# Kernel optimization log

Measured on AMD Instinct MI355X. Metric: run time of the kernel, lower is better.

Reference implementation:

```python
import jax, jax.numpy as jnp
import numpy as np

B, L, D, H, F, NL = 112, 128, 768, 12, 3072, 3
E = D // H  # head dim = 64
BN_EPS = 1e-5


def _bn(x, gamma, beta):
    # torch BatchNorm1d applied on x.permute(0,2,1): per-channel (d_model) stats over batch+seq
    mean = jnp.mean(x, axis=(0, 1), keepdims=True)
    var = jnp.var(x, axis=(0, 1), keepdims=True)
    return (x - mean) * jax.lax.rsqrt(var + BN_EPS) * gamma + beta


def setup_inputs() -> dict:
    key = jax.random.key(0)
    ks = jax.random.split(key, 10)
    s = 0.02
    inp = {
        "x": jax.random.normal(ks[0], (B, L, D), jnp.float32),
        "attn_bias": jax.random.normal(ks[1], (B, L, L, H), jnp.float32) * 0.1,
        "Wq": jax.random.normal(ks[2], (NL, D, D), jnp.float32) * s,
        "bq": jnp.zeros((NL, D), jnp.float32),
        "Wk": jax.random.normal(ks[3], (NL, D, D), jnp.float32) * s,
        "bk": jnp.zeros((NL, D), jnp.float32),
        "Wv": jax.random.normal(ks[4], (NL, D, D), jnp.float32) * s,
        "bv": jnp.zeros((NL, D), jnp.float32),
        "Wo": jax.random.normal(ks[5], (NL, D, D), jnp.float32) * s,
        "bo": jnp.zeros((NL, D), jnp.float32),
        "W1": jax.random.normal(ks[6], (NL, F, D), jnp.float32) * s,  # conv1 k=1 == Linear
        "b1": jnp.zeros((NL, F), jnp.float32),
        "W2": jax.random.normal(ks[7], (NL, D, F), jnp.float32) * s,  # conv2 k=1 == Linear
        "b2": jnp.zeros((NL, D), jnp.float32),
        "g1": jnp.ones((NL, D), jnp.float32),
        "be1": jnp.zeros((NL, D), jnp.float32),
        "g2": jnp.ones((NL, D), jnp.float32),
        "be2": jnp.zeros((NL, D), jnp.float32),
        "gf": jnp.ones((D,), jnp.float32),
        "bef": jnp.zeros((D,), jnp.float32),
    }
    return inp


def reference(x, attn_bias, Wq, bq, Wk, bk, Wv, bv, Wo, bo,
              W1, b1, W2, b2, g1, be1, g2, be2, gf, bef):
    scale = 1.0 / float(np.sqrt(E))
    bias_bhls = jnp.transpose(attn_bias, (0, 3, 1, 2))  # [B,H,L,S]
    for l in range(NL):
        q = (x @ Wq[l].T + bq[l]).reshape(B, L, H, E)
        k = (x @ Wk[l].T + bk[l]).reshape(B, L, H, E)
        v = (x @ Wv[l].T + bv[l]).reshape(B, L, H, E)
        scores = jnp.einsum('blhe,bshe->bhls', q, k)  # O(L^2) score tensor
        A = jax.nn.softmax(scores * scale + bias_bhls, axis=-1)
        V = jnp.einsum('bhls,bshd->blhd', A, v).reshape(B, L, D)
        new_x = V @ Wo[l].T + bo[l]
        x = _bn(x + new_x, g1[l], be1[l])
        y = jax.nn.gelu(x @ W1[l].T + b1[l], approximate=False)
        y = y @ W2[l].T + b2[l]
        x = _bn(x + y, g2[l], be2[l])
    return _bn(x, gf, bef)  # Encoder final BatchNorm1d(d_model)
```

## Files before the change

kernel.cpp:

```cpp
#include <hip/hip_runtime.h>

#define NB 112
#define SEQ 128
#define DM 768
#define NH 12
#define HD 64
#define FF 3072
#define NLAYER 3
#define MTOK (NB*SEQ)
#define QKVN (3*DM)
#define HEADTOT (NB*NH)
#define QSZ ((size_t)HEADTOT*SEQ*HD)

typedef unsigned short u16;
typedef __attribute__((ext_vector_type(8))) short short8;
typedef __attribute__((ext_vector_type(4))) float f32x4;
typedef __attribute__((ext_vector_type(4))) unsigned short us4;

__device__ __forceinline__ u16 f2bf(float f){
  unsigned u = __builtin_bit_cast(unsigned, f);
  u += 0x7FFFu + ((u >> 16) & 1u);
  return (u16)(u >> 16);
}
__device__ __forceinline__ float bf2f(u16 b){
  unsigned u = ((unsigned)b) << 16;
  return __builtin_bit_cast(float, u);
}
__device__ __forceinline__ unsigned cvt_pk_bf16(float lo, float hi){
  unsigned r;
  asm("v_cvt_pk_bf16_f32 %0, %1, %2" : "=v"(r) : "v"(lo), "v"(hi));
  return r;
}
__device__ __forceinline__ float gelu_t(float x){
  const float t = -1.5957691216057308f * x * __builtin_fmaf(0.044715f, x*x, 1.0f);
  return __fdividef(x, 1.0f + __expf(t));
}

__device__ __forceinline__ void gl_lds16(const void* g, void* l){
  __builtin_amdgcn_global_load_lds((const __attribute__((address_space(1))) unsigned*)g,
                                   (__attribute__((address_space(3))) unsigned*)l, 16, 0, 0);
}

template<int EPI>
__global__ __launch_bounds__(512, 2)
void gemm_bt(const u16* __restrict__ A, const u16* __restrict__ W,
             const float* __restrict__ bias, u16* __restrict__ obf,
             float* __restrict__ of32, const u16* __restrict__ res,
             float* __restrict__ p1, float* __restrict__ p2,
             int M, int N, int K, int Nt, int TPB)
{
  __shared__ __align__(16) char smem[131072];
  const int tid = threadIdx.x;
  const int w = tid >> 6, lane = tid & 63;
  const int wm = w >> 2, wn = w & 3;
  const int fr = lane & 15, fg = lane >> 4;
  const int fko = fg * 8;
  const int grid = gridDim.x;
  const int q8 = grid >> 3, r8 = grid & 7;
  const int xcd = blockIdx.x & 7, pos = blockIdx.x >> 3;
  const int start = xcd < r8 ? xcd * (q8 + 1) : r8 * (q8 + 1) + (xcd - r8) * q8;
  const int swz = start + pos;
  const int nt = K >> 6;
  const int tot = TPB * nt;
  const int l3 = lane >> 3;
  const int k16s = ((lane & 7) ^ l3) * 8;
  int rowAK[2][2], rowBK[2][2];
  #pragma unroll
  for (int mh = 0; mh < 2; mh++)
    #pragma unroll
    for (int j = 0; j < 2; j++)
      rowAK[mh][j] = (mh*64 + j*128 + w*8 + l3) * K;
  #pragma unroll
  for (int h = 0; h < 2; h++)
    #pragma unroll
    for (int j = 0; j < 2; j++)
      rowBK[h][j] = (h*128 + (w + j*8)*8 + l3) * K;

  auto stA2 = [&](int bb, int mh, int soff) {
    const u16* g0 = A + (size_t)soff + rowAK[mh][0] + k16s;
    const u16* g1 = A + (size_t)soff + rowAK[mh][1] + k16s;
    char* d = smem + bb*65536 + (mh*64 + w*8)*128;
    gl_lds16(g0, d);
    gl_lds16(g1, d + 16384);
  };
  auto stB2 = [&](int bb, int h, int soff) {
    const u16* g0 = W + (size_t)soff + rowBK[h][0] + k16s;
    const u16* g1 = W + (size_t)soff + rowBK[h][1] + k16s;
    char* d = smem + bb*65536 + 32768 + (h*128 + w*8)*128;
    gl_lds16(g0, d);
    gl_lds16(g1, d + 8192);
  };
  const int axor = (fr & 7) << 4;
  auto rdA2 = [&](int bb, int mh, int kh, int mf) -> short8 {
    const int row = wm*128 + mh*64 + mf*16 + fr;
    return *(const short8*)(smem + bb*65536 + row*128 + (((kh*32 + fko)*2) ^ axor));
  };
  auto rdB2 = [&](int bb, int kh, int nf) -> short8 {
    const int row = wn*64 + nf*16 + fr;
    return *(const short8*)(smem + bb*65536 + 32768 + row*128 + (((kh*32 + fko)*2) ^ axor));
  };
  auto coord = [&](int r, int& bm, int& bn) {
    const int lin = swz * TPB + r;
    const int mI = lin / Nt;
    bm = mI * 256; bn = (lin - mI * Nt) * 256;
  };

  f32x4 acc[8][4] = {};

  auto epi = [&](int bm, int bn) {
    float bs[4] = {0,0,0,0}, bq[4] = {0,0,0,0};
    #pragma unroll
    for (int mi = 0; mi < 8; mi++) {
      #pragma unroll
      for (int ni = 0; ni < 4; ni++) {
        const int c = bn + wn*64 + ni*16 + fr;
        const int r0 = bm + wm*128 + (mi>>2)*64 + (mi&3)*16 + fg*4;
        const float bc = bias[c];
        float v[4];
        #pragma unroll
        for (int j = 0; j < 4; j++) v[j] = acc[mi][ni][j] + bc;
        if constexpr (EPI == 1) {
          #pragma unroll
          for (int j = 0; j < 4; j++) v[j] = gelu_t(v[j]);
          const unsigned p01 = cvt_pk_bf16(v[0], v[1]);
          const unsigned p23 = cvt_pk_bf16(v[2], v[3]);
          u16* d = obf + (size_t)r0 * N + c;
          d[0] = (u16)p01; d[N] = (u16)(p01 >> 16);
          d[2*N] = (u16)p23; d[3*N] = (u16)(p23 >> 16);
        } else if constexpr (EPI == 2) {
          #pragma unroll
          for (int j = 0; j < 4; j++) {
            const float y = v[j] + bf2f(res[(size_t)(r0+j) * N + c]);
            of32[(size_t)(r0+j) * N + c] = y;
            bs[ni] += y; bq[ni] += y * y;
          }
        } else {
          const int which = c / DM;
          const int cc = c - which * DM;
          const int hh = cc >> 6, e = cc & 63;
          const int bb = r0 >> 7, l = r0 & 127;
          const unsigned p01 = cvt_pk_bf16(v[0], v[1]);
          const unsigned p23 = cvt_pk_bf16(v[2], v[3]);
          u16* d = obf + (size_t)which * QSZ + ((size_t)(bb*NH + hh) * SEQ + l) * HD + e;
          d[0] = (u16)p01; d[HD] = (u16)(p01 >> 16);
          d[2*HD] = (u16)p23; d[3*HD] = (u16)(p23 >> 16);
        }
        acc[mi][ni] = (f32x4){0.f, 0.f, 0.f, 0.f};
      }
    }
    if constexpr (EPI == 2) {
      const int mIdx = bm >> 8;
      #pragma unroll
      for (int ni = 0; ni < 4; ni++) {
        float s = bs[ni], qq = bq[ni];
        s  += __shfl_xor(s, 16);  s  += __shfl_xor(s, 32);
        qq += __shfl_xor(qq, 16); qq += __shfl_xor(qq, 32);
        if (fg == 0) {
          const int c = bn + wn*64 + ni*16 + fr;
          p1[(mIdx*2 + wm) * N + c] = s;
          p2[(mIdx*2 + wm) * N + c] = qq;
        }
      }
    }
  };

  int r0t = 0, kt0 = 0, bm0, bn0; coord(0, bm0, bn0);
  int r1 = 0, kt1 = 1, bm1 = bm0, bn1 = bn0;
  int r2 = 0, kt2 = 2, bm2 = bm0;
  if (kt2 >= nt) { kt2 -= nt; r2 = 1; int d; if (r2 < TPB) coord(r2, bm2, d); }

  stA2(0, 0, bm0*K); stA2(0, 1, bm0*K);
  stB2(0, 0, bn0*K); stB2(0, 1, bn0*K);
  if (tot > 1) stA2(1, 0, bm1*K + kt1*64);
  asm volatile("s_waitcnt vmcnt(2)" ::: "memory");
  __builtin_amdgcn_s_barrier();

  short8 a0[4], a1[4], bk0[4], bk1[4];
  for (int it = 0; it < tot; ++it) {
    const int bufc = it & 1, nb = bufc ^ 1;
    const bool st1 = (it + 1 < tot), st2 = (it + 2 < tot);
    const int sB1 = bn1*K + kt1*64;
    const int sA1 = bm1*K + kt1*64;
    const int sA2 = bm2*K + kt2*64;
    #pragma unroll
    for (int i = 0; i < 4; i++) a0[i] = rdA2(bufc, 0, 0, i);
    #pragma unroll
    for (int i = 0; i < 4; i++) a1[i] = rdA2(bufc, 0, 1, i);
    #pragma unroll
    for (int i = 0; i < 4; i++) bk0[i] = rdB2(bufc, 0, i);
    #pragma unroll
    for (int i = 0; i < 4; i++) bk1[i] = rdB2(bufc, 1, i);
    if (st1) { stB2(nb, 0, sB1); stB2(nb, 1, sB1); }
    __builtin_amdgcn_s_barrier();
    asm volatile("s_waitcnt lgkmcnt(0)" ::: "memory");
    __builtin_amdgcn_sched_barrier(0);
    __builtin_amdgcn_s_setprio(1);
    #pragma unroll
    for (int mi = 0; mi < 4; mi++)
      #pragma unroll
      for (int ni = 0; ni < 4; ni++)
        acc[mi][ni] = __builtin_amdgcn_mfma_f32_16x16x32_bf16(a0[mi], bk0[ni], acc[mi][ni], 0, 0, 0);
    #pragma unroll
    for (int mi = 0; mi < 4; mi++)
      #pragma unroll
      for (int ni = 0; ni < 4; ni++)
        acc[mi][ni] = __builtin_amdgcn_mfma_f32_16x16x32_bf16(a1[mi], bk1[ni], acc[mi][ni], 0, 0, 0);
    __builtin_amdgcn_s_setprio(0);
    if (st1) { asm volatile("s_waitcnt vmcnt(4)" ::: "memory"); }
    else     { asm volatile("s_waitcnt vmcnt(0)" ::: "memory"); }
    __builtin_amdgcn_s_barrier();
    #pragma unroll
    for (int i = 0; i < 4; i++) a0[i] = rdA2(bufc, 1, 0, i);
    #pragma unroll
    for (int i = 0; i < 4; i++) a1[i] = rdA2(bufc, 1, 1, i);
    if (st2) stA2(bufc, 0, sA2);
    if (st1) stA2(nb, 1, sA1);
    __builtin_amdgcn_s_barrier();
    asm volatile("s_waitcnt lgkmcnt(0)" ::: "memory");
    __builtin_amdgcn_sched_barrier(0);
    __builtin_amdgcn_s_setprio(1);
    #pragma unroll
    for (int mi = 0; mi < 4; mi++)
      #pragma unroll
      for (int ni = 0; ni < 4; ni++)
        acc[4+mi][ni] = __builtin_amdgcn_mfma_f32_16x16x32_bf16(a0[mi], bk0[ni], acc[4+mi][ni], 0, 0, 0);
    #pragma unroll
    for (int mi = 0; mi < 4; mi++)
      #pragma unroll
      for (int ni = 0; ni < 4; ni++)
        acc[4+mi][ni] = __builtin_amdgcn_mfma_f32_16x16x32_bf16(a1[mi], bk1[ni], acc[4+mi][ni], 0, 0, 0);
    __builtin_amdgcn_s_setprio(0);
    if (st2)      { asm volatile("s_waitcnt vmcnt(4)" ::: "memory"); }
    else if (st1) { asm volatile("s_waitcnt vmcnt(2)" ::: "memory"); }
    __builtin_amdgcn_s_barrier();
    if (kt0 == nt - 1) {
      epi(bm0, bn0);
      kt0 = 0; r0t++;
      if (r0t < TPB) coord(r0t, bm0, bn0);
    } else kt0++;
    kt1++; if (kt1 == nt) { kt1 = 0; r1++; if (r1 < TPB) coord(r1, bm1, bn1); }
    kt2++; if (kt2 == nt) { kt2 = 0; r2++; if (r2 < TPB) { int d; coord(r2, bm2, d); } }
  }
}

__global__ __launch_bounds__(256)
void attn_kernel(const u16* __restrict__ qkvb, const u16* __restrict__ biasT,
                 u16* __restrict__ ab)
{
  const int h = blockIdx.x, b = blockIdx.y;
  const int tid = threadIdx.x, w = tid >> 6, lane = tid & 63;
  const int bh = b * NH + h;
  const u16* qp = qkvb + (size_t)bh * SEQ * HD;
  const u16* kp = qkvb + QSZ + (size_t)bh * SEQ * HD;
  const u16* vp = qkvb + 2 * QSZ + (size_t)bh * SEQ * HD;
  __shared__ __align__(16) u16 vT[HD * 136];
  __shared__ __align__(16) u16 P[SEQ * 136];
  {
    const int s = tid & 127, half = tid >> 7;
    #pragma unroll
    for (int rr = 0; rr < 4; rr++) {
      const int e0 = half * 32 + rr * 8;
      short8 v8 = *(const short8*)&vp[s * HD + e0];
      #pragma unroll
      for (int j = 0; j < 8; j++) vT[(e0 + j) * 136 + s] = (u16)v8[j];
    }
  }
  const int fr = lane & 15, fg = lane >> 4;
  f32x4 sacc[2][8] = {};
  #pragma unroll
  for (int ks = 0; ks < 2; ks++) {
    const int k0 = ks * 32 + fg * 8;
    short8 qf[2], kf[8];
    #pragma unroll
    for (int mi = 0; mi < 2; mi++) qf[mi] = *(const short8*)&qp[(w*32 + mi*16 + fr) * HD + k0];
    #pragma unroll
    for (int ni = 0; ni < 8; ni++) kf[ni] = *(const short8*)&kp[(ni*16 + fr) * HD + k0];
    #pragma unroll
    for (int mi = 0; mi < 2; mi++)
      #pragma unroll
      for (int ni = 0; ni < 8; ni++)
        sacc[mi][ni] = __builtin_amdgcn_mfma_f32_16x16x32_bf16(qf[mi], kf[ni], sacc[mi][ni], 0, 0, 0);
  }
  const u16* bt = biasT + (size_t)bh * SEQ * SEQ;
  #pragma unroll
  for (int mi = 0; mi < 2; mi++) {
    #pragma unroll
    for (int j = 0; j < 4; j++) {
      const int l = w*32 + mi*16 + fg*4 + j;
      float vals[8];
      float mx = -1e30f;
      #pragma unroll
      for (int ni = 0; ni < 8; ni++) {
        vals[ni] = sacc[mi][ni][j] * 0.125f + bf2f(bt[l * SEQ + ni*16 + fr]);
        mx = fmaxf(mx, vals[ni]);
      }
      #pragma unroll
      for (int d = 1; d < 16; d <<= 1) mx = fmaxf(mx, __shfl_xor(mx, d));
      float sum = 0.f;
      #pragma unroll
      for (int ni = 0; ni < 8; ni++) { vals[ni] = __expf(vals[ni] - mx); sum += vals[ni]; }
      #pragma unroll
      for (int d = 1; d < 16; d <<= 1) sum += __shfl_xor(sum, d);
      const float inv = 1.0f / sum;
      #pragma unroll
      for (int ni = 0; ni < 8; ni++) P[l * 136 + ni*16 + fr] = f2bf(vals[ni] * inv);
    }
  }
  __syncthreads();
  f32x4 oacc[2][4] = {};
  #pragma unroll
  for (int ss = 0; ss < 4; ss++) {
    const int s0 = ss * 32 + fg * 8;
    short8 pf[2], vf[4];
    #pragma unroll
    for (int mi = 0; mi < 2; mi++) pf[mi] = *(const short8*)&P[(w*32 + mi*16 + fr) * 136 + s0];
    #pragma unroll
    for (int ei = 0; ei < 4; ei++) vf[ei] = *(const short8*)&vT[(ei*16 + fr) * 136 + s0];
    #pragma unroll
    for (int mi = 0; mi < 2; mi++)
      #pragma unroll
      for (int ei = 0; ei < 4; ei++)
        oacc[mi][ei] = __builtin_amdgcn_mfma_f32_16x16x32_bf16(pf[mi], vf[ei], oacc[mi][ei], 0, 0, 0);
  }
  #pragma unroll
  for (int mi = 0; mi < 2; mi++)
    #pragma unroll
    for (int ei = 0; ei < 4; ei++)
      #pragma unroll
      for (int j = 0; j < 4; j++) {
        const int r = b * SEQ + w*32 + mi*16 + fg*4 + j;
        const int c = h * HD + ei*16 + fr;
        ab[(size_t)r * DM + c] = f2bf(oacc[mi][ei][j]);
      }
}

template<bool FINAL>
__global__ __launch_bounds__(256)
void bn_final(const float* __restrict__ p1, const float* __restrict__ p2,
              const float* __restrict__ ga, const float* __restrict__ be,
              const float* __restrict__ gb, const float* __restrict__ beb,
              float* __restrict__ sc, float* __restrict__ sh)
{
  const int c = blockIdx.x * 256 + threadIdx.x;
  float s = 0, q = 0;
  for (int i = 0; i < 112; i++) { s += p1[i * DM + c]; q += p2[i * DM + c]; }
  const float mean = s * (1.0f / MTOK);
  const float var = q * (1.0f / MTOK) - mean * mean;
  const float rstd = rsqrtf(var + 1e-5f);
  if constexpr (!FINAL) {
    const float g = ga[c] * rstd;
    sc[c] = g;
    sh[c] = be[c] - mean * g;
  } else {
    const float sc2 = ga[c] * rstd;
    const float sh2 = be[c] - mean * sc2;
    const float varf = sc2 * sc2 * var;
    const float meanf = sc2 * mean + sh2;
    const float scf = gb[c] * rsqrtf(varf + 1e-5f);
    const float shf = beb[c] - meanf * scf;
    sc[c] = scf * sc2;
    sh[c] = scf * sh2 + shf;
  }
}

template<int MODE>
__global__ __launch_bounds__(256)
void bn_apply(const float* __restrict__ xi, const float* __restrict__ sc,
              const float* __restrict__ sh, float* __restrict__ xo, u16* __restrict__ xb)
{
  const int i = blockIdx.x * 256 + threadIdx.x;
  const int c0 = (i % (DM / 8)) * 2;
  float4 v0 = ((const float4*)xi)[i*2];
  float4 v1 = ((const float4*)xi)[i*2 + 1];
  const float4 s0 = ((const float4*)sc)[c0];
  const float4 s1 = ((const float4*)sc)[c0 + 1];
  const float4 h0 = ((const float4*)sh)[c0];
  const float4 h1 = ((const float4*)sh)[c0 + 1];
  float y0x = __builtin_fmaf(v0.x, s0.x, h0.x), y0y = __builtin_fmaf(v0.y, s0.y, h0.y);
  float y0z = __builtin_fmaf(v0.z, s0.z, h0.z), y0w = __builtin_fmaf(v0.w, s0.w, h0.w);
  float y1x = __builtin_fmaf(v1.x, s1.x, h1.x), y1y = __builtin_fmaf(v1.y, s1.y, h1.y);
  float y1z = __builtin_fmaf(v1.z, s1.z, h1.z), y1w = __builtin_fmaf(v1.w, s1.w, h1.w);
  if constexpr (MODE == 1) {
    ((float4*)xo)[i*2]     = (float4){y0x, y0y, y0z, y0w};
    ((float4*)xo)[i*2 + 1] = (float4){y1x, y1y, y1z, y1w};
  } else {
    short8 r;
    unsigned pA = cvt_pk_bf16(y0x, y0y), pB = cvt_pk_bf16(y0z, y0w);
    unsigned pC = cvt_pk_bf16(y1x, y1y), pD = cvt_pk_bf16(y1z, y1w);
    r[0] = (short)(u16)pA; r[1] = (short)(u16)(pA >> 16);
    r[2] = (short)(u16)pB; r[3] = (short)(u16)(pB >> 16);
    r[4] = (short)(u16)pC; r[5] = (short)(u16)(pC >> 16);
    r[6] = (short)(u16)pD; r[7] = (short)(u16)(pD >> 16);
    *(short8*)&xb[(size_t)i * 8] = r;
  }
}

__global__ __launch_bounds__(256)
void conv_bf16(const float* __restrict__ s, u16* __restrict__ d, int n8)
{
  const int i = blockIdx.x * 256 + threadIdx.x;
  if (i >= n8) return;
  float4 v0 = ((const float4*)s)[i*2];
  float4 v1 = ((const float4*)s)[i*2 + 1];
  short8 r;
  unsigned pA = cvt_pk_bf16(v0.x, v0.y), pB = cvt_pk_bf16(v0.z, v0.w);
  unsigned pC = cvt_pk_bf16(v1.x, v1.y), pD = cvt_pk_bf16(v1.z, v1.w);
  r[0] = (short)(u16)pA; r[1] = (short)(u16)(pA >> 16);
  r[2] = (short)(u16)pB; r[3] = (short)(u16)(pB >> 16);
  r[4] = (short)(u16)pC; r[5] = (short)(u16)(pC >> 16);
  r[6] = (short)(u16)pD; r[7] = (short)(u16)(pD >> 16);
  *(short8*)&d[(size_t)i * 8] = r;
}

__global__ __launch_bounds__(256)
void conv_qkvw(const float* __restrict__ wq, const float* __restrict__ wk,
               const float* __restrict__ wv, u16* __restrict__ d)
{
  const int i = blockIdx.x * 256 + threadIdx.x;
  const int per = QKVN * DM / 8;
  const int l = i / per;
  const int rem = i - l * per;
  const int r = rem / (DM / 8);
  const int cv = rem - r * (DM / 8);
  const float* srcrow;
  if (r < DM)          srcrow = wq + ((size_t)l * DM + r) * DM;
  else if (r < 2 * DM) srcrow = wk + ((size_t)l * DM + (r - DM)) * DM;
  else                 srcrow = wv + ((size_t)l * DM + (r - 2 * DM)) * DM;
  float4 v0 = ((const float4*)srcrow)[cv*2];
  float4 v1 = ((const float4*)srcrow)[cv*2 + 1];
  short8 o;
  unsigned pA = cvt_pk_bf16(v0.x, v0.y), pB = cvt_pk_bf16(v0.z, v0.w);
  unsigned pC = cvt_pk_bf16(v1.x, v1.y), pD = cvt_pk_bf16(v1.z, v1.w);
  o[0] = (short)(u16)pA; o[1] = (short)(u16)(pA >> 16);
  o[2] = (short)(u16)pB; o[3] = (short)(u16)(pB >> 16);
  o[4] = (short)(u16)pC; o[5] = (short)(u16)(pC >> 16);
  o[6] = (short)(u16)pD; o[7] = (short)(u16)(pD >> 16);
  *(short8*)&d[(size_t)i * 8] = o;
}

__global__ __launch_bounds__(256)
void conv_bias_qkv(const float* __restrict__ bq, const float* __restrict__ bk,
                   const float* __restrict__ bv, float* __restrict__ d)
{
  const int i = blockIdx.x * 256 + threadIdx.x;
  const int l = i / QKVN;
  const int r = i - l * QKVN;
  float v;
  if (r < DM)          v = bq[l * DM + r];
  else if (r < 2 * DM) v = bk[l * DM + r - DM];
  else                 v = bv[l * DM + r - 2 * DM];
  d[i] = v;
}

__global__ __launch_bounds__(256)
void bias_tr(const float* __restrict__ src, u16* __restrict__ dst)
{
  const int l = blockIdx.x, b = blockIdx.y;
  __shared__ float row[SEQ * NH];
  const float* s = src + ((size_t)b * SEQ + l) * SEQ * NH;
  for (int i = threadIdx.x; i < SEQ * NH; i += 256) row[i] = s[i];
  __syncthreads();
  for (int i = threadIdx.x; i < SEQ * NH; i += 256) {
    const int h = i >> 7, ss = i & 127;
    dst[((size_t)(b * NH + h) * SEQ + l) * SEQ + ss] = f2bf(row[ss * NH + h]);
  }
}

extern "C" void kernel_launch(void* const* d_in, const int* in_sizes, int n_in,
                              void* d_out, int out_size, void* d_ws, size_t ws_size,
                              hipStream_t stream)
{
  const float* x    = (const float*)d_in[0];
  const float* abia = (const float*)d_in[1];
  const float* Wq   = (const float*)d_in[2];
  const float* bq   = (const float*)d_in[3];
  const float* Wk   = (const float*)d_in[4];
  const float* bk   = (const float*)d_in[5];
  const float* Wv   = (const float*)d_in[6];
  const float* bv   = (const float*)d_in[7];
  const float* Wo   = (const float*)d_in[8];
  const float* bo   = (const float*)d_in[9];
  const float* W1   = (const float*)d_in[10];
  const float* b1   = (const float*)d_in[11];
  const float* W2   = (const float*)d_in[12];
  const float* b2   = (const float*)d_in[13];
  const float* g1   = (const float*)d_in[14];
  const float* be1  = (const float*)d_in[15];
  const float* g2   = (const float*)d_in[16];
  const float* be2  = (const float*)d_in[17];
  const float* gf   = (const float*)d_in[18];
  const float* bef  = (const float*)d_in[19];
  float* out = (float*)d_out;

  char* ws = (char*)d_ws;
  size_t off = 0;
  auto alloc = [&](size_t n) -> char* {
    char* p = ws + off;
    off = (off + n + 255) & ~(size_t)255;
    return p;
  };
  u16*  wqkv  = (u16*)alloc((size_t)3 * QKVN * DM * 2);
  u16*  wo    = (u16*)alloc((size_t)3 * DM * DM * 2);
  u16*  w1    = (u16*)alloc((size_t)3 * FF * DM * 2);
  u16*  w2    = (u16*)alloc((size_t)3 * DM * FF * 2);
  float* bqkv = (float*)alloc((size_t)3 * QKVN * 4);
  u16*  xb    = (u16*)alloc((size_t)MTOK * DM * 2);
  u16*  ab    = (u16*)alloc((size_t)MTOK * DM * 2);
  u16*  big   = (u16*)alloc((size_t)MTOK * FF * 2);
  u16*  biasT = (u16*)alloc((size_t)HEADTOT * SEQ * SEQ * 2);
  float* p1   = (float*)alloc((size_t)112 * DM * 4);
  float* p2   = (float*)alloc((size_t)112 * DM * 4);
  float* sc   = (float*)alloc(DM * 4);
  float* sh   = (float*)alloc(DM * 4);
  if (off > ws_size) return;

  conv_qkvw<<<2592, 256, 0, stream>>>(Wq, Wk, Wv, wqkv);
  conv_bf16<<<864, 256, 0, stream>>>(Wo, wo, 3 * DM * DM / 8);
  conv_bf16<<<3456, 256, 0, stream>>>(W1, w1, 3 * FF * DM / 8);
  conv_bf16<<<3456, 256, 0, stream>>>(W2, w2, 3 * DM * FF / 8);
  conv_bias_qkv<<<27, 256, 0, stream>>>(bq, bk, bv, bqkv);
  bias_tr<<<dim3(SEQ, NB), 256, 0, stream>>>(abia, biasT);
  conv_bf16<<<MTOK * DM / 8 / 256, 256, 0, stream>>>(x, xb, MTOK * DM / 8);

  auto gemm = [&](int epi, const u16* Ap, const u16* Wp, const float* bp,
                  u16* ob, float* o32, const u16* rs, int M, int N, int K) {
    const int Nt = N / 256;
    const int tiles = (M / 256) * Nt;
    const int tpb = (tiles + 255) / 256;
    const int grid = tiles / tpb;
    if (epi == 1)
      gemm_bt<1><<<grid, 512, 0, stream>>>(Ap, Wp, bp, ob, o32, rs, p1, p2, M, N, K, Nt, tpb);
    else if (epi == 2)
      gemm_bt<2><<<grid, 512, 0, stream>>>(Ap, Wp, bp, ob, o32, rs, p1, p2, M, N, K, Nt, tpb);
    else
      gemm_bt<3><<<grid, 512, 0, stream>>>(Ap, Wp, bp, ob, o32, rs, p1, p2, M, N, K, Nt, tpb);
  };

  for (int l = 0; l < NLAYER; l++) {
    gemm(3, xb, wqkv + (size_t)l * QKVN * DM, bqkv + l * QKVN, big, nullptr, nullptr,
         MTOK, QKVN, DM);
    attn_kernel<<<dim3(NH, NB), 256, 0, stream>>>(big, biasT, ab);
    gemm(2, ab, wo + (size_t)l * DM * DM, bo + l * DM, nullptr, out, xb,
         MTOK, DM, DM);
    bn_final<false><<<3, 256, 0, stream>>>(p1, p2, g1 + l * DM, be1 + l * DM,
                                           nullptr, nullptr, sc, sh);
    bn_apply<0><<<MTOK * DM / 8 / 256, 256, 0, stream>>>(out, sc, sh, nullptr, xb);
    gemm(1, xb, w1 + (size_t)l * FF * DM, b1 + l * FF, big, nullptr, nullptr,
         MTOK, FF, DM);
    gemm(2, big, w2 + (size_t)l * DM * FF, b2 + l * DM, nullptr, out, xb,
         MTOK, DM, FF);
    if (l < NLAYER - 1) {
      bn_final<false><<<3, 256, 0, stream>>>(p1, p2, g2 + l * DM, be2 + l * DM,
                                             nullptr, nullptr, sc, sh);
      bn_apply<0><<<MTOK * DM / 8 / 256, 256, 0, stream>>>(out, sc, sh, nullptr, xb);
    } else {
      bn_final<true><<<3, 256, 0, stream>>>(p1, p2, g2 + l * DM, be2 + l * DM,
                                            gf, bef, sc, sh);
      bn_apply<1><<<MTOK * DM / 8 / 256, 256, 0, stream>>>(out, sc, sh, out, nullptr);
    }
  }
}
```

Baseline: 1.146 ms.

## Triple-buffer A tiles in GEMM LDS to cut per-iteration barriers

Restructures the GEMM main loop from a double-buffered scheme with split A half-tile loads and three barriers per iteration to a three-slot A ring plus two-slot B ring, issuing full-tile async loads once per iteration with one barrier. LDS grows to 160KB, so launch bounds drop to one block of 512 threads per CU. This aims to remove barrier stalls and deepen prefetch, at the cost of halving occupancy and less latency hiding across blocks.

New measurement: 1.132 ms (median of 2 runs). No clear change (-1.2%).

```diff
diff --git a/kernel.cpp b/kernel.cpp
--- a/kernel.cpp
+++ b/kernel.cpp
@@ -42,14 +42,14 @@
 }
 
 template<int EPI>
-__global__ __launch_bounds__(512, 2)
+__global__ __launch_bounds__(512, 1)
 void gemm_bt(const u16* __restrict__ A, const u16* __restrict__ W,
              const float* __restrict__ bias, u16* __restrict__ obf,
              float* __restrict__ of32, const u16* __restrict__ res,
              float* __restrict__ p1, float* __restrict__ p2,
              int M, int N, int K, int Nt, int TPB)
 {
-  __shared__ __align__(16) char smem[131072];
+  __shared__ __align__(16) char smem[163840];
   const int tid = threadIdx.x;
   const int w = tid >> 6, lane = tid & 63;
   const int wm = w >> 2, wn = w & 3;
@@ -76,28 +76,30 @@
     for (int j = 0; j < 2; j++)
       rowBK[h][j] = (h*128 + (w + j*8)*8 + l3) * K;
 
-  auto stA2 = [&](int bb, int mh, int soff) {
-    const u16* g0 = A + (size_t)soff + rowAK[mh][0] + k16s;
-    const u16* g1 = A + (size_t)soff + rowAK[mh][1] + k16s;
-    char* d = smem + bb*65536 + (mh*64 + w*8)*128;
-    gl_lds16(g0, d);
-    gl_lds16(g1, d + 16384);
-  };
-  auto stB2 = [&](int bb, int h, int soff) {
-    const u16* g0 = W + (size_t)soff + rowBK[h][0] + k16s;
-    const u16* g1 = W + (size_t)soff + rowBK[h][1] + k16s;
-    char* d = smem + bb*65536 + 32768 + (h*128 + w*8)*128;
-    gl_lds16(g0, d);
-    gl_lds16(g1, d + 8192);
+  auto stA = [&](int s, int soff) {
+    #pragma unroll
+    for (int mh = 0; mh < 2; mh++) {
+      char* d = smem + s*32768 + (mh*64 + w*8)*128;
+      gl_lds16(A + (size_t)soff + rowAK[mh][0] + k16s, d);
+      gl_lds16(A + (size_t)soff + rowAK[mh][1] + k16s, d + 16384);
+    }
+  };
+  auto stB = [&](int s, int soff) {
+    #pragma unroll
+    for (int h = 0; h < 2; h++) {
+      char* d = smem + 98304 + s*32768 + (h*128 + w*8)*128;
+      gl_lds16(W + (size_t)soff + rowBK[h][0] + k16s, d);
+      gl_lds16(W + (size_t)soff + rowBK[h][1] + k16s, d + 8192);
+    }
   };
   const int axor = (fr & 7) << 4;
-  auto rdA2 = [&](int bb, int mh, int kh, int mf) -> short8 {
+  auto rdA2 = [&](int s, int mh, int kh, int mf) -> short8 {
     const int row = wm*128 + mh*64 + mf*16 + fr;
-    return *(const short8*)(smem + bb*65536 + row*128 + (((kh*32 + fko)*2) ^ axor));
-  };
-  auto rdB2 = [&](int bb, int kh, int nf) -> short8 {
+    return *(const short8*)(smem + s*32768 + row*128 + (((kh*32 + fko)*2) ^ axor));
+  };
+  auto rdB2 = [&](int s, int kh, int nf) -> short8 {
     const int row = wn*64 + nf*16 + fr;
-    return *(const short8*)(smem + bb*65536 + 32768 + row*128 + (((kh*32 + fko)*2) ^ axor));
+    return *(const short8*)(smem + 98304 + s*32768 + row*128 + (((kh*32 + fko)*2) ^ axor));
   };
   auto coord = [&](int r, int& bm, int& bn) {
     const int lin = swz * TPB + r;
@@ -169,29 +171,31 @@
   int r2 = 0, kt2 = 2, bm2 = bm0;
   if (kt2 >= nt) { kt2 -= nt; r2 = 1; int d; if (r2 < TPB) coord(r2, bm2, d); }
 
-  stA2(0, 0, bm0*K); stA2(0, 1, bm0*K);
-  stB2(0, 0, bn0*K); stB2(0, 1, bn0*K);
-  if (tot > 1) stA2(1, 0, bm1*K + kt1*64);
-  asm volatile("s_waitcnt vmcnt(2)" ::: "memory");
+  stA(0, bm0*K + kt0*64);
+  stB(0, bn0*K + kt0*64);
+  if (tot > 1) stA(1, bm1*K + kt1*64);
+  asm volatile("s_waitcnt vmcnt(4)" ::: "memory");
   __builtin_amdgcn_s_barrier();
 
   short8 a0[4], a1[4], bk0[4], bk1[4];
+  int bufA = 0;
   for (int it = 0; it < tot; ++it) {
-    const int bufc = it & 1, nb = bufc ^ 1;
+    const int bufB = it & 1;
+    int slA2 = bufA + 2; if (slA2 >= 3) slA2 -= 3;
+    const int slB1 = bufB ^ 1;
     const bool st1 = (it + 1 < tot), st2 = (it + 2 < tot);
     const int sB1 = bn1*K + kt1*64;
-    const int sA1 = bm1*K + kt1*64;
     const int sA2 = bm2*K + kt2*64;
     #pragma unroll
-    for (int i = 0; i < 4; i++) a0[i] = rdA2(bufc, 0, 0, i);
-    #pragma unroll
-    for (int i = 0; i < 4; i++) a1[i] = rdA2(bufc, 0, 1, i);
-    #pragma unroll
-    for (int i = 0; i < 4; i++) bk0[i] = rdB2(bufc, 0, i);
-    #pragma unroll
-    for (int i = 0; i < 4; i++) bk1[i] = rdB2(bufc, 1, i);
-    if (st1) { stB2(nb, 0, sB1); stB2(nb, 1, sB1); }
-    __builtin_amdgcn_s_barrier();
+    for (int i = 0; i < 4; i++) a0[i] = rdA2(bufA, 0, 0, i);
+    #pragma unroll
+    for (int i = 0; i < 4; i++) a1[i] = rdA2(bufA, 0, 1, i);
+    #pragma unroll
+    for (int i = 0; i < 4; i++) bk0[i] = rdB2(bufB, 0, i);
+    #pragma unroll
+    for (int i = 0; i < 4; i++) bk1[i] = rdB2(bufB, 1, i);
+    if (st1) stB(slB1, sB1);
+    if (st2) stA(slA2, sA2);
     asm volatile("s_waitcnt lgkmcnt(0)" ::: "memory");
     __builtin_amdgcn_sched_barrier(0);
     __builtin_amdgcn_s_setprio(1);
@@ -206,16 +210,10 @@
       for (int ni = 0; ni < 4; ni++)
         acc[mi][ni] = __builtin_amdgcn_mfma_f32_16x16x32_bf16(a1[mi], bk1[ni], acc[mi][ni], 0, 0, 0);
     __builtin_amdgcn_s_setprio(0);
-    if (st1) { asm volatile("s_waitcnt vmcnt(4)" ::: "memory"); }
-    else     { asm volatile("s_waitcnt vmcnt(0)" ::: "memory"); }
-    __builtin_amdgcn_s_barrier();
-    #pragma unroll
-    for (int i = 0; i < 4; i++) a0[i] = rdA2(bufc, 1, 0, i);
-    #pragma unroll
-    for (int i = 0; i < 4; i++) a1[i] = rdA2(bufc, 1, 1, i);
-    if (st2) stA2(bufc, 0, sA2);
-    if (st1) stA2(nb, 1, sA1);
-    __builtin_amdgcn_s_barrier();
+    #pragma unroll
+    for (int i = 0; i < 4; i++) a0[i] = rdA2(bufA, 1, 0, i);
+    #pragma unroll
+    for (int i = 0; i < 4; i++) a1[i] = rdA2(bufA, 1, 1, i);
     asm volatile("s_waitcnt lgkmcnt(0)" ::: "memory");
     __builtin_amdgcn_sched_barrier(0);
     __builtin_amdgcn_s_setprio(1);
@@ -231,7 +229,7 @@
         acc[4+mi][ni] = __builtin_amdgcn_mfma_f32_16x16x32_bf16(a1[mi], bk1[ni], acc[4+mi][ni], 0, 0, 0);
     __builtin_amdgcn_s_setprio(0);
     if (st2)      { asm volatile("s_waitcnt vmcnt(4)" ::: "memory"); }
-    else if (st1) { asm volatile("s_waitcnt vmcnt(2)" ::: "memory"); }
+    else if (st1) { asm volatile("s_waitcnt vmcnt(0)" ::: "memory"); }
     __builtin_amdgcn_s_barrier();
     if (kt0 == nt - 1) {
       epi(bm0, bn0);
@@ -240,6 +238,7 @@
     } else kt0++;
     kt1++; if (kt1 == nt) { kt1 = 0; r1++; if (r1 < TPB) coord(r1, bm1, bn1); }
     kt2++; if (kt2 == nt) { kt2 = 0; r2++; if (r2 < TPB) { int d; coord(r2, bm2, d); } }
+    bufA++; if (bufA == 3) bufA = 0;
   }
 }
 
```
